# Performance work log

Hardware: AMD Instinct MI355X
Metric: run time of the kernel (lower is better)

Reference implementation:

```python
import jax, jax.numpy as jnp
import numpy as np

N = 50000      # nodes
E = 800000     # edges (avg degree 16)
IN = 64        # in_channels
OUT = 64       # out_channels
K = 3          # Chebyshev order
LAM = 2.0      # lambda_max for sym normalization


def setup_inputs() -> dict:
    key = jax.random.key(0)
    ks = jax.random.split(key, 16)
    s_in = 1.0 / np.sqrt(IN)
    s_out = 1.0 / np.sqrt(OUT)
    inp = {
        "X": jax.random.normal(ks[0], (N, IN), jnp.float32),
        "edge_index": jax.random.randint(ks[1], (2, E), 0, N, dtype=jnp.int64),
        "edge_weight": jax.random.uniform(ks[2], (E,), jnp.float32),
        # six ChebConv weight stacks [K, in, out] and biases [out]
        "W_xz": jax.random.normal(ks[3], (K, IN, OUT), jnp.float32) * s_in,
        "W_hz": jax.random.normal(ks[4], (K, OUT, OUT), jnp.float32) * s_out,
        "W_xr": jax.random.normal(ks[5], (K, IN, OUT), jnp.float32) * s_in,
        "W_hr": jax.random.normal(ks[6], (K, OUT, OUT), jnp.float32) * s_out,
        "W_xh": jax.random.normal(ks[7], (K, IN, OUT), jnp.float32) * s_in,
        "W_hh": jax.random.normal(ks[8], (K, OUT, OUT), jnp.float32) * s_out,
        "b_xz": jnp.zeros((OUT,), jnp.float32),
        "b_hz": jnp.zeros((OUT,), jnp.float32),
        "b_xr": jnp.zeros((OUT,), jnp.float32),
        "b_hr": jnp.zeros((OUT,), jnp.float32),
        "b_xh": jnp.zeros((OUT,), jnp.float32),
        "b_hh": jnp.zeros((OUT,), jnp.float32),
    }
    return inp


def _cheb_norm(edge_index, edge_weight):
    # PyG ChebConv __norm__ with sym normalization, lambda_max = 2:
    # L_hat = (2/lam) * (I - D^-1/2 A D^-1/2) - I
    src, dst = edge_index[0], edge_index[1]
    deg = jax.ops.segment_sum(edge_weight, src, num_segments=N)
    dinv = jnp.where(deg > 0, jax.lax.rsqrt(jnp.where(deg > 0, deg, 1.0)), 0.0)
    w_off = -(2.0 / LAM) * edge_weight * dinv[src] * dinv[dst]
    diag = 2.0 / LAM - 1.0  # 0 when lambda_max == 2
    return src, dst, w_off, diag


def _spmm(x, src, dst, w_off, diag):
    # y[i] = sum_{e: dst[e]=i} w_off[e] * x[src[e]] + diag * x[i]
    msg = w_off[:, None] * x[src]
    return jax.ops.segment_sum(msg, dst, num_segments=N) + diag * x


def _cheb_conv(x, W, b, src, dst, w_off, diag):
    Tx0 = x
    out = Tx0 @ W[0]
    Tx1 = _spmm(Tx0, src, dst, w_off, diag)
    out = out + Tx1 @ W[1]
    for k in range(2, K):
        Tx2 = 2.0 * _spmm(Tx1, src, dst, w_off, diag) - Tx0
        out = out + Tx2 @ W[k]
        Tx0, Tx1 = Tx1, Tx2
    return out + b


def reference(X, edge_index, edge_weight,
              W_xz, W_hz, W_xr, W_hr, W_xh, W_hh,
              b_xz, b_hz, b_xr, b_hr, b_xh, b_hh):
    src, dst, w_off, diag = _cheb_norm(edge_index, edge_weight)
    cheb = lambda x, W, b: _cheb_conv(x, W, b, src, dst, w_off, diag)
    H = jnp.zeros((N, OUT), X.dtype)  # _set_hidden_state with H=None
    Z = jax.nn.sigmoid(cheb(X, W_xz, b_xz) + cheb(H, W_hz, b_hz))
    R = jax.nn.sigmoid(cheb(X, W_xr, b_xr) + cheb(H, W_hr, b_hr))
    H_tilde = jnp.tanh(cheb(X, W_xh, b_xh) + cheb(H * R, W_hh, b_hh))
    H_new = Z * H + (1.0 - Z) * H_tilde
    return H_new
```

## Files before the change

### kernel.cpp

```cpp
#include <hip/hip_runtime.h>


#define N_NODES 50000
#define E_EDGES 800000
#define NC 64
#define BSH 6
#define BUKN 64
#define NBUK 782
#define EPB 2048
#define NBLK 391

#define OFF_CV       0
#define OFF_ROWSTART 1600000
#define OFF_TOTD     1650016
#define OFF_BASED    1650800
#define OFF_TOTS     1651584
#define OFF_BASES    1652368
#define OFF_TX1      1653152
#define OFF_RECD     1653152
#define OFF_DINV     3253152
#define OFF_CNTD     3303168
#define OFF_TX2      4853152
#define OFF_RECS     4853152
#define OFF_CNTS     6453152
#define OFF_WB       8053152

typedef __attribute__((ext_vector_type(8))) short bf16x8;
typedef __attribute__((ext_vector_type(4))) float f32x4;

__device__ __forceinline__ unsigned bf16rne(float x) {
    unsigned u = __float_as_uint(x);
    return (u + 0x7fffu + ((u >> 16) & 1u)) >> 16;
}

__global__ __launch_bounds__(256) void k_hist(const int* __restrict__ ei,
        int* __restrict__ cntD, int* __restrict__ cntS,
        const float* __restrict__ Wz, const float* __restrict__ Wh,
        short* __restrict__ WB) {
    int t = threadIdx.x, blk = blockIdx.x;
    if (blk >= NBLK) {
        int mg = blk - NBLK;
        int m = mg >> 1, g = mg & 1;
        const float* W = (g ? Wh : Wz) + m * 4096;
        #pragma unroll
        for (int r = 0; r < 16; ++r) {
            int idx = r * 256 + t;
            int c = idx >> 6, o = idx & 63;
            float x = W[idx];
            unsigned hi = bf16rne(x);
            float fhi = __uint_as_float(hi << 16);
            unsigned lo = bf16rne(x - fhi);
            WB[(mg * 2 + 0) * 4096 + o * 64 + c] = (short)hi;
            WB[(mg * 2 + 1) * 4096 + o * 64 + c] = (short)lo;
        }
        return;
    }
    __shared__ int hD[NBUK], hS[NBUK];
    for (int b = t; b < NBUK; b += 256) { hD[b] = 0; hS[b] = 0; }
    __syncthreads();
    int e0 = blk * EPB;
    #pragma unroll
    for (int i = 0; i < 8; ++i) {
        int e = e0 + i * 256 + t;
        if (e < E_EDGES) {
            atomicAdd(&hS[ei[e] >> BSH], 1);
            atomicAdd(&hD[ei[E_EDGES + e] >> BSH], 1);
        }
    }
    __syncthreads();
    for (int b = t; b < NBUK; b += 256) {
        cntD[b * NBLK + blk] = hD[b];
        cntS[b * NBLK + blk] = hS[b];
    }
}

__global__ __launch_bounds__(256) void k_scanPB(int* __restrict__ cntD,
        int* __restrict__ cntS, int* __restrict__ totD, int* __restrict__ totS) {
    __shared__ int s[512];
    int t = threadIdx.x;
    int row = blockIdx.x; int* cnt; int* tot;
    if (row < NBUK) { cnt = cntD; tot = totD; }
    else            { row -= NBUK; cnt = cntS; tot = totS; }
    int v0 = (t < NBLK) ? cnt[row * NBLK + t] : 0;
    int v1 = (256 + t < NBLK) ? cnt[row * NBLK + 256 + t] : 0;
    s[t] = v0; s[256 + t] = v1;
    __syncthreads();
    for (int off = 1; off < 512; off <<= 1) {
        int a = (t >= off) ? s[t - off] : 0;
        int b = (256 + t >= off) ? s[256 + t - off] : 0;
        __syncthreads();
        s[t] += a; s[256 + t] += b;
        __syncthreads();
    }
    if (t < NBLK) cnt[row * NBLK + t] = s[t] - v0;
    if (256 + t < NBLK) cnt[row * NBLK + 256 + t] = s[256 + t] - v1;
    if (t == 0) tot[row] = s[511];
}

__global__ __launch_bounds__(256) void k_scanTot(int* __restrict__ totD,
        int* __restrict__ baseD, int* __restrict__ totS, int* __restrict__ baseS) {
    __shared__ int s[1024];
    int t = threadIdx.x;
    int* tot  = blockIdx.x ? totS  : totD;
    int* base = blockIdx.x ? baseS : baseD;
    int v[4];
    #pragma unroll
    for (int q = 0; q < 4; ++q) {
        int i = q * 256 + t;
        v[q] = (i < NBUK) ? tot[i] : 0;
        s[i] = v[q];
    }
    __syncthreads();
    for (int off = 1; off < 1024; off <<= 1) {
        int a[4];
        #pragma unroll
        for (int q = 0; q < 4; ++q) {
            int i = q * 256 + t;
            a[q] = (i >= off) ? s[i - off] : 0;
        }
        __syncthreads();
        #pragma unroll
        for (int q = 0; q < 4; ++q) s[q * 256 + t] += a[q];
        __syncthreads();
    }
    #pragma unroll
    for (int q = 0; q < 4; ++q) {
        int i = q * 256 + t;
        if (i < NBUK) base[i] = s[i] - v[q];
    }
}

__global__ __launch_bounds__(256) void k_scatter(const int* __restrict__ ei,
        const float* __restrict__ ew, const int* __restrict__ offD,
        const int* __restrict__ offS, const int* __restrict__ baseD,
        const int* __restrict__ baseS, long long* __restrict__ recD,
        long long* __restrict__ recS) {
    __shared__ int curD[NBUK], curS[NBUK];
    int t = threadIdx.x, blk = blockIdx.x;
    for (int b = t; b < NBUK; b += 256) {
        curD[b] = baseD[b] + offD[b * NBLK + blk];
        curS[b] = baseS[b] + offS[b * NBLK + blk];
    }
    __syncthreads();
    int e0 = blk * EPB;
    #pragma unroll
    for (int i = 0; i < 8; ++i) {
        int e = e0 + i * 256 + t;
        if (e < E_EDGES) {
            int sN = ei[e], dN = ei[E_EDGES + e];
            long long wb = (long long)(unsigned)__float_as_uint(ew[e]) << 32;
            int pD = atomicAdd(&curD[dN >> BSH], 1);
            recD[pD] = wb | (unsigned)((sN << BSH) | (dN & (BUKN - 1)));
            int pS = atomicAdd(&curS[sN >> BSH], 1);
            recS[pS] = wb | (unsigned)(sN & (BUKN - 1));
        }
    }
}

__global__ __launch_bounds__(256) void k_deg(const long long* __restrict__ recS,
        const int* __restrict__ totS, const int* __restrict__ baseS,
        float* __restrict__ dinv) {
    __shared__ float degL[BUKN];
    int t = threadIdx.x, b = blockIdx.x;
    if (t < BUKN) degL[t] = 0.f;
    __syncthreads();
    int st = baseS[b], n = totS[b];
    for (int i = t; i < n; i += 256) {
        long long r = recS[st + i];
        atomicAdd(&degL[(int)(r & (BUKN - 1))], __uint_as_float((unsigned)(r >> 32)));
    }
    __syncthreads();
    if (t < BUKN) {
        int node = b * BUKN + t;
        if (node < N_NODES) {
            float dg = degL[t];
            dinv[node] = dg > 0.f ? rsqrtf(dg) : 0.f;
        }
    }
}

__global__ __launch_bounds__(256) void k_csr(const long long* __restrict__ recD,
        const int* __restrict__ totD, const int* __restrict__ baseD,
        const float* __restrict__ dinv, long long* __restrict__ cv,
        int* __restrict__ row_start) {
    __shared__ int cnt[BUKN], cur[BUKN];
    __shared__ float dL[BUKN];
    int t = threadIdx.x, b = blockIdx.x;
    if (t < BUKN) {
        cnt[t] = 0;
        int node = b * BUKN + t;
        dL[t] = (node < N_NODES) ? dinv[node] : 0.f;
    }
    __syncthreads();
    int st = baseD[b], n = totD[b];
    for (int i = t; i < n; i += 256)
        atomicAdd(&cnt[(int)(recD[st + i] & (BUKN - 1))], 1);
    __syncthreads();
    if (t < BUKN) {
        int x = cnt[t];
        int orig = x;
        #pragma unroll
        for (int off = 1; off < BUKN; off <<= 1) {
            int v = __shfl_up(x, off, 64);
            if ((t & 63) >= off) x += v;
        }
        cur[t] = x - orig;
        int node = b * BUKN + t;
        if (node < N_NODES) row_start[node] = st + (x - orig);
    }
    if (b == 0 && t == 0) row_start[N_NODES] = E_EDGES;
    __syncthreads();
    for (int i = t; i < n; i += 256) {
        long long r = recD[st + i];
        int m = (int)(r & 0xffffffffLL);
        float w = __uint_as_float((unsigned)(r >> 32));
        int rr = m & (BUKN - 1);
        int sN = m >> BSH;
        float val = -w * dinv[sN] * dL[rr];
        int pos = st + atomicAdd(&cur[rr], 1);
        cv[pos] = ((long long)__float_as_int(val) << 32) | (unsigned)sN;
    }
}

template<int SCALE, int SUB>
__global__ __launch_bounds__(256) void k_spmm(
        const int* __restrict__ row_start, const long long* __restrict__ cv,
        const float* __restrict__ xin, const float* __restrict__ xprev,
        float* __restrict__ out) {
    int wid = (blockIdx.x << 2) + (threadIdx.x >> 6);
    int l = threadIdx.x & 63;
    if (wid >= N_NODES) return;
    int start = row_start[wid];
    int end   = row_start[wid + 1];
    int sub = l >> 4;
    int q   = l & 15;
    float4 acc = make_float4(0.f, 0.f, 0.f, 0.f);
    for (int j = start; j < end; j += 8) {
        int jA = j + sub;
        int jB = j + 4 + sub;
        long long pA = (jA < end) ? cv[jA] : 0LL;
        long long pB = (jB < end) ? cv[jB] : 0LL;
        float4 xA = *(const float4*)&xin[(size_t)(unsigned)(pA & 0xffffffffLL) * NC + q * 4];
        float4 xB = *(const float4*)&xin[(size_t)(unsigned)(pB & 0xffffffffLL) * NC + q * 4];
        float vA = __int_as_float((int)(pA >> 32));
        float vB = __int_as_float((int)(pB >> 32));
        acc.x = fmaf(vA, xA.x, acc.x);
        acc.y = fmaf(vA, xA.y, acc.y);
        acc.z = fmaf(vA, xA.z, acc.z);
        acc.w = fmaf(vA, xA.w, acc.w);
        acc.x = fmaf(vB, xB.x, acc.x);
        acc.y = fmaf(vB, xB.y, acc.y);
        acc.z = fmaf(vB, xB.z, acc.z);
        acc.w = fmaf(vB, xB.w, acc.w);
    }
    #pragma unroll
    for (int m = 16; m <= 32; m <<= 1) {
        acc.x += __shfl_xor(acc.x, m, 64);
        acc.y += __shfl_xor(acc.y, m, 64);
        acc.z += __shfl_xor(acc.z, m, 64);
        acc.w += __shfl_xor(acc.w, m, 64);
    }
    if (sub == 0) {
        float4 r;
        r.x = (float)SCALE * acc.x;
        r.y = (float)SCALE * acc.y;
        r.z = (float)SCALE * acc.z;
        r.w = (float)SCALE * acc.w;
        if (SUB) {
            float4 xo = *(const float4*)&xprev[(size_t)wid * NC + q * 4];
            r.x -= xo.x; r.y -= xo.y; r.z -= xo.z; r.w -= xo.w;
        }
        *(float4*)&out[(size_t)wid * NC + q * 4] = r;
    }
}

__global__ __launch_bounds__(256) void k_gru(
        const float* __restrict__ X, const float* __restrict__ Tx1,
        const float* __restrict__ Tx2, const short* __restrict__ WB,
        const float* __restrict__ bxz, const float* __restrict__ bhz,
        const float* __restrict__ bxh, const float* __restrict__ bhh,
        float* __restrict__ out) {
    __shared__ short Ahi[64 * 64];
    __shared__ short Alo[64 * 64];
    int tid = threadIdx.x;
    int l = tid & 63;
    int w = tid >> 6;
    int node0 = blockIdx.x * 64;

    f32x4 accz[4], acch[4];
    #pragma unroll
    for (int mt = 0; mt < 4; ++mt) {
        accz[mt] = (f32x4){0.f, 0.f, 0.f, 0.f};
        acch[mt] = (f32x4){0.f, 0.f, 0.f, 0.f};
    }

    const float* ins[3] = {X, Tx1, Tx2};
    #pragma unroll 1
    for (int m = 0; m < 3; ++m) {
        __syncthreads();
        const float* ip = ins[m];
        #pragma unroll
        for (int r = 0; r < 4; ++r) {
            int fidx = r * 256 + tid;
            int n = fidx >> 4, c4 = fidx & 15;
            int gn = node0 + n;
            float4 v = make_float4(0.f, 0.f, 0.f, 0.f);
            if (gn < N_NODES) v = *(const float4*)&ip[(size_t)gn * 64 + c4 * 4];
            unsigned h0 = bf16rne(v.x), h1 = bf16rne(v.y),
                     h2 = bf16rne(v.z), h3 = bf16rne(v.w);
            unsigned q0 = bf16rne(v.x - __uint_as_float(h0 << 16));
            unsigned q1 = bf16rne(v.y - __uint_as_float(h1 << 16));
            unsigned q2 = bf16rne(v.z - __uint_as_float(h2 << 16));
            unsigned q3 = bf16rne(v.w - __uint_as_float(h3 << 16));
            int kk = (c4 * 4) ^ ((n & 7) << 3);
            *(uint2*)&Ahi[n * 64 + kk] = make_uint2(h0 | (h1 << 16), h2 | (h3 << 16));
            *(uint2*)&Alo[n * 64 + kk] = make_uint2(q0 | (q1 << 16), q2 | (q3 << 16));
        }
        __syncthreads();
        const short* wbm = WB + m * 4 * 4096;
        #pragma unroll
        for (int kt = 0; kt < 2; ++kt) {
            int k0 = kt * 32 + (l >> 4) * 8;
            bf16x8 ah[4], al[4];
            #pragma unroll
            for (int mt = 0; mt < 4; ++mt) {
                int row = mt * 16 + (l & 15);
                int kk = k0 ^ ((row & 7) << 3);
                ah[mt] = *(const bf16x8*)&Ahi[row * 64 + kk];
                al[mt] = *(const bf16x8*)&Alo[row * 64 + kk];
            }
            int o = w * 16 + (l & 15);
            {
                bf16x8 bh_ = *(const bf16x8*)&wbm[0 * 4096 + o * 64 + k0];
                bf16x8 bl_ = *(const bf16x8*)&wbm[1 * 4096 + o * 64 + k0];
                #pragma unroll
                for (int mt = 0; mt < 4; ++mt) {
                    accz[mt] = __builtin_amdgcn_mfma_f32_16x16x32_bf16(ah[mt], bh_, accz[mt], 0, 0, 0);
                    accz[mt] = __builtin_amdgcn_mfma_f32_16x16x32_bf16(ah[mt], bl_, accz[mt], 0, 0, 0);
                    accz[mt] = __builtin_amdgcn_mfma_f32_16x16x32_bf16(al[mt], bh_, accz[mt], 0, 0, 0);
                }
            }
            {
                bf16x8 bh_ = *(const bf16x8*)&wbm[2 * 4096 + o * 64 + k0];
                bf16x8 bl_ = *(const bf16x8*)&wbm[3 * 4096 + o * 64 + k0];
                #pragma unroll
                for (int mt = 0; mt < 4; ++mt) {
                    acch[mt] = __builtin_amdgcn_mfma_f32_16x16x32_bf16(ah[mt], bh_, acch[mt], 0, 0, 0);
                    acch[mt] = __builtin_amdgcn_mfma_f32_16x16x32_bf16(ah[mt], bl_, acch[mt], 0, 0, 0);
                    acch[mt] = __builtin_amdgcn_mfma_f32_16x16x32_bf16(al[mt], bh_, acch[mt], 0, 0, 0);
                }
            }
        }
    }

    int o = w * 16 + (l & 15);
    float bz = bxz[o] + bhz[o];
    float bh = bxh[o] + bhh[o];
    #pragma unroll
    for (int mt = 0; mt < 4; ++mt) {
        #pragma unroll
        for (int r = 0; r < 4; ++r) {
            int node = node0 + mt * 16 + (l >> 4) * 4 + r;
            if (node < N_NODES) {
                float z = accz[mt][r] + bz;
                float h = acch[mt][r] + bh;
                float sig = 1.f / (1.f + __expf(-z));
                float e2 = __expf(-2.f * h);
                float th = (1.f - e2) / (1.f + e2);
                out[(size_t)node * 64 + o] = (1.f - sig) * th;
            }
        }
    }
}

extern "C" void kernel_launch(void* const* d_in, const int* in_sizes, int n_in,
                              void* d_out, int out_size, void* d_ws, size_t ws_size,
                              hipStream_t stream) {
    const float* X   = (const float*)d_in[0];
    const int*   ei  = (const int*)d_in[1];
    const float* ew  = (const float*)d_in[2];
    const float* Wxz = (const float*)d_in[3];
    const float* Wxh = (const float*)d_in[7];
    const float* bxz = (const float*)d_in[9];
    const float* bhz = (const float*)d_in[10];
    const float* bxh = (const float*)d_in[13];
    const float* bhh = (const float*)d_in[14];
    float* out = (float*)d_out;

    float* ws_f = (float*)d_ws;
    int*   ws_i = (int*)d_ws;

    long long* cv       = (long long*)(ws_i + OFF_CV);
    int*       rowstart = ws_i + OFF_ROWSTART;
    int*       totD     = ws_i + OFF_TOTD;
    int*       baseD    = ws_i + OFF_BASED;
    int*       totS     = ws_i + OFF_TOTS;
    int*       baseS    = ws_i + OFF_BASES;
    float*     tx1      = ws_f + OFF_TX1;
    long long* recD     = (long long*)(ws_i + OFF_RECD);
    float*     dinv     = ws_f + OFF_DINV;
    int*       cntD     = ws_i + OFF_CNTD;
    float*     tx2      = ws_f + OFF_TX2;
    long long* recS     = (long long*)(ws_i + OFF_RECS);
    int*       cntS     = ws_i + OFF_CNTS;
    short*     WB       = (short*)(ws_i + OFF_WB);

    const int TB = 256;
    k_hist<<<NBLK + 6, TB, 0, stream>>>(ei, cntD, cntS, Wxz, Wxh, WB);
    k_scanPB<<<2 * NBUK, TB, 0, stream>>>(cntD, cntS, totD, totS);
    k_scanTot<<<2, TB, 0, stream>>>(totD, baseD, totS, baseS);
    k_scatter<<<NBLK, TB, 0, stream>>>(ei, ew, cntD, cntS, baseD, baseS, recD, recS);
    k_deg<<<NBUK, TB, 0, stream>>>(recS, totS, baseS, dinv);
    k_csr<<<NBUK, TB, 0, stream>>>(recD, totD, baseD, dinv, cv, rowstart);

    k_spmm<1, 0><<<(N_NODES + 3) / 4, TB, 0, stream>>>(rowstart, cv, X, X, tx1);
    k_spmm<2, 1><<<(N_NODES + 3) / 4, TB, 0, stream>>>(rowstart, cv, tx1, X, tx2);

    k_gru<<<NBUK, TB, 0, stream>>>(X, tx1, tx2, WB, bxz, bhz, bxh, bhh, out);
}
```

Measured before the change: 147.1 us.

## Factor degree normalization out of CSR and pre-split bf16 operands in producers

Stores raw edge weights in the CSR and applies the D^-1/2 scaling algebraically: the source side is prescaled (xs = dinv*X, u1 = dinv*Tx1) and the destination side is applied at the end of each SpMM row, so k_csr no longer does random dinv gathers. The hi/lo bf16 split of X, Tx1 and Tx2 moves into the producing kernels (k_degx, k_spmm), and k_gru now reads those pre-split operands straight from global memory instead of converting through LDS with barriers. k_csr also caches bucket records in LDS to avoid rereading them. The cost is extra workspace and extra global writes for the split arrays and prescaled copies, and the MFMA A-operand loads in k_gru become strided global reads.

```diff
diff --git a/kernel.cpp b/kernel.cpp
--- a/kernel.cpp
+++ b/kernel.cpp
@@ -7,8 +7,10 @@
 #define BSH 6
 #define BUKN 64
 #define NBUK 782
+#define NPADROW 50048
 #define EPB 2048
 #define NBLK 391
+#define CSR_CAP 1536
 
 #define OFF_CV       0
 #define OFF_ROWSTART 1600000
@@ -16,14 +18,20 @@
 #define OFF_BASED    1650800
 #define OFF_TOTS     1651584
 #define OFF_BASES    1652368
-#define OFF_TX1      1653152
-#define OFF_RECD     1653152
-#define OFF_DINV     3253152
-#define OFF_CNTD     3303168
-#define OFF_TX2      4853152
-#define OFF_RECS     4853152
-#define OFF_CNTS     6453152
-#define OFF_WB       8053152
+#define OFF_XS       1653152
+#define OFF_U1       4853152
+#define OFF_RECD     8053152
+#define OFF_RECS     9653152
+#define OFF_DINV     11253152
+#define OFF_CNTD     11303200
+#define OFF_CNTS     11608962
+#define OFF_WB       11914724
+#define OFF_XHI      11939300
+#define OFF_XLO      13540836
+#define OFF_T1HI     15142372
+#define OFF_T1LO     16743908
+#define OFF_T2HI     18345444
+#define OFF_T2LO     19946980
 
 typedef __attribute__((ext_vector_type(8))) short bf16x8;
 typedef __attribute__((ext_vector_type(4))) float f32x4;
@@ -157,10 +165,11 @@
     }
 }
 
-__global__ __launch_bounds__(256) void k_deg(const long long* __restrict__ recS,
+__global__ __launch_bounds__(256) void k_degx(const long long* __restrict__ recS,
         const int* __restrict__ totS, const int* __restrict__ baseS,
-        float* __restrict__ dinv) {
-    __shared__ float degL[BUKN];
+        const float* __restrict__ X, float* __restrict__ dinv,
+        float* __restrict__ xs, short* __restrict__ xhi, short* __restrict__ xlo) {
+    __shared__ float degL[BUKN], dinvL[BUKN];
     int t = threadIdx.x, b = blockIdx.x;
     if (t < BUKN) degL[t] = 0.f;
     __syncthreads();
@@ -172,29 +181,50 @@
     __syncthreads();
     if (t < BUKN) {
         int node = b * BUKN + t;
-        if (node < N_NODES) {
-            float dg = degL[t];
-            dinv[node] = dg > 0.f ? rsqrtf(dg) : 0.f;
-        }
+        float dg = degL[t];
+        float dv = (node < N_NODES && dg > 0.f) ? rsqrtf(dg) : 0.f;
+        dinvL[t] = dv;
+        if (node < N_NODES) dinv[node] = dv;
+    }
+    __syncthreads();
+    #pragma unroll
+    for (int it = 0; it < 4; ++it) {
+        int fidx = it * 256 + t;
+        int rl = fidx >> 4, c4 = fidx & 15;
+        int gn = b * BUKN + rl;
+        float4 v = make_float4(0.f, 0.f, 0.f, 0.f);
+        if (gn < N_NODES) v = *(const float4*)&X[(size_t)gn * 64 + c4 * 4];
+        float dv = dinvL[rl];
+        if (gn < N_NODES) {
+            float4 sv = make_float4(dv * v.x, dv * v.y, dv * v.z, dv * v.w);
+            *(float4*)&xs[(size_t)gn * 64 + c4 * 4] = sv;
+        }
+        unsigned h0 = bf16rne(v.x), h1 = bf16rne(v.y),
+                 h2 = bf16rne(v.z), h3 = bf16rne(v.w);
+        unsigned q0 = bf16rne(v.x - __uint_as_float(h0 << 16));
+        unsigned q1 = bf16rne(v.y - __uint_as_float(h1 << 16));
+        unsigned q2 = bf16rne(v.z - __uint_as_float(h2 << 16));
+        unsigned q3 = bf16rne(v.w - __uint_as_float(h3 << 16));
+        *(uint2*)&xhi[(size_t)gn * 64 + c4 * 4] = make_uint2(h0 | (h1 << 16), h2 | (h3 << 16));
+        *(uint2*)&xlo[(size_t)gn * 64 + c4 * 4] = make_uint2(q0 | (q1 << 16), q2 | (q3 << 16));
     }
 }
 
 __global__ __launch_bounds__(256) void k_csr(const long long* __restrict__ recD,
         const int* __restrict__ totD, const int* __restrict__ baseD,
-        const float* __restrict__ dinv, long long* __restrict__ cv,
-        int* __restrict__ row_start) {
+        long long* __restrict__ cv, int* __restrict__ row_start) {
+    __shared__ long long recL[CSR_CAP];
     __shared__ int cnt[BUKN], cur[BUKN];
-    __shared__ float dL[BUKN];
     int t = threadIdx.x, b = blockIdx.x;
-    if (t < BUKN) {
-        cnt[t] = 0;
-        int node = b * BUKN + t;
-        dL[t] = (node < N_NODES) ? dinv[node] : 0.f;
-    }
+    if (t < BUKN) cnt[t] = 0;
     __syncthreads();
     int st = baseD[b], n = totD[b];
-    for (int i = t; i < n; i += 256)
-        atomicAdd(&cnt[(int)(recD[st + i] & (BUKN - 1))], 1);
+    bool fits = (n <= CSR_CAP);
+    for (int i = t; i < n; i += 256) {
+        long long r = recD[st + i];
+        if (fits) recL[i] = r;
+        atomicAdd(&cnt[(int)(r & (BUKN - 1))], 1);
+    }
     __syncthreads();
     if (t < BUKN) {
         int x = cnt[t];
@@ -211,22 +241,21 @@
     if (b == 0 && t == 0) row_start[N_NODES] = E_EDGES;
     __syncthreads();
     for (int i = t; i < n; i += 256) {
-        long long r = recD[st + i];
+        long long r = fits ? recL[i] : recD[st + i];
         int m = (int)(r & 0xffffffffLL);
-        float w = __uint_as_float((unsigned)(r >> 32));
         int rr = m & (BUKN - 1);
         int sN = m >> BSH;
-        float val = -w * dinv[sN] * dL[rr];
         int pos = st + atomicAdd(&cur[rr], 1);
-        cv[pos] = ((long long)__float_as_int(val) << 32) | (unsigned)sN;
-    }
-}
-
-template<int SCALE, int SUB>
+        cv[pos] = (r & 0xffffffff00000000LL) | (unsigned)sN;
+    }
+}
+
+template<int PASS>
 __global__ __launch_bounds__(256) void k_spmm(
         const int* __restrict__ row_start, const long long* __restrict__ cv,
-        const float* __restrict__ xin, const float* __restrict__ xprev,
-        float* __restrict__ out) {
+        const float* __restrict__ gsrc, const float* __restrict__ X,
+        const float* __restrict__ dinv, float* __restrict__ u1,
+        short* __restrict__ phi, short* __restrict__ plo) {
     int wid = (blockIdx.x << 2) + (threadIdx.x >> 6);
     int l = threadIdx.x & 63;
     if (wid >= N_NODES) return;
@@ -235,23 +264,20 @@
     int sub = l >> 4;
     int q   = l & 15;
     float4 acc = make_float4(0.f, 0.f, 0.f, 0.f);
+    #pragma unroll 2
     for (int j = start; j < end; j += 8) {
         int jA = j + sub;
         int jB = j + 4 + sub;
         long long pA = (jA < end) ? cv[jA] : 0LL;
         long long pB = (jB < end) ? cv[jB] : 0LL;
-        float4 xA = *(const float4*)&xin[(size_t)(unsigned)(pA & 0xffffffffLL) * NC + q * 4];
-        float4 xB = *(const float4*)&xin[(size_t)(unsigned)(pB & 0xffffffffLL) * NC + q * 4];
+        float4 xA = *(const float4*)&gsrc[(size_t)(unsigned)(pA & 0xffffffffLL) * NC + q * 4];
+        float4 xB = *(const float4*)&gsrc[(size_t)(unsigned)(pB & 0xffffffffLL) * NC + q * 4];
         float vA = __int_as_float((int)(pA >> 32));
         float vB = __int_as_float((int)(pB >> 32));
-        acc.x = fmaf(vA, xA.x, acc.x);
-        acc.y = fmaf(vA, xA.y, acc.y);
-        acc.z = fmaf(vA, xA.z, acc.z);
-        acc.w = fmaf(vA, xA.w, acc.w);
-        acc.x = fmaf(vB, xB.x, acc.x);
-        acc.y = fmaf(vB, xB.y, acc.y);
-        acc.z = fmaf(vB, xB.z, acc.z);
-        acc.w = fmaf(vB, xB.w, acc.w);
+        acc.x = fmaf(vA, xA.x, acc.x); acc.y = fmaf(vA, xA.y, acc.y);
+        acc.z = fmaf(vA, xA.z, acc.z); acc.w = fmaf(vA, xA.w, acc.w);
+        acc.x = fmaf(vB, xB.x, acc.x); acc.y = fmaf(vB, xB.y, acc.y);
+        acc.z = fmaf(vB, xB.z, acc.z); acc.w = fmaf(vB, xB.w, acc.w);
     }
     #pragma unroll
     for (int m = 16; m <= 32; m <<= 1) {
@@ -261,27 +287,37 @@
         acc.w += __shfl_xor(acc.w, m, 64);
     }
     if (sub == 0) {
+        float dv = dinv[wid];
         float4 r;
-        r.x = (float)SCALE * acc.x;
-        r.y = (float)SCALE * acc.y;
-        r.z = (float)SCALE * acc.z;
-        r.w = (float)SCALE * acc.w;
-        if (SUB) {
-            float4 xo = *(const float4*)&xprev[(size_t)wid * NC + q * 4];
-            r.x -= xo.x; r.y -= xo.y; r.z -= xo.z; r.w -= xo.w;
-        }
-        *(float4*)&out[(size_t)wid * NC + q * 4] = r;
+        if (PASS == 1) {
+            r.x = -dv * acc.x; r.y = -dv * acc.y;
+            r.z = -dv * acc.z; r.w = -dv * acc.w;
+            *(float4*)&u1[(size_t)wid * NC + q * 4] =
+                make_float4(dv * r.x, dv * r.y, dv * r.z, dv * r.w);
+        } else {
+            const float4 xo = *(const float4*)&X[(size_t)wid * NC + q * 4];
+            r.x = -2.f * dv * acc.x - xo.x; r.y = -2.f * dv * acc.y - xo.y;
+            r.z = -2.f * dv * acc.z - xo.z; r.w = -2.f * dv * acc.w - xo.w;
+        }
+        unsigned h0 = bf16rne(r.x), h1 = bf16rne(r.y),
+                 h2 = bf16rne(r.z), h3 = bf16rne(r.w);
+        unsigned q0 = bf16rne(r.x - __uint_as_float(h0 << 16));
+        unsigned q1 = bf16rne(r.y - __uint_as_float(h1 << 16));
+        unsigned q2 = bf16rne(r.z - __uint_as_float(h2 << 16));
+        unsigned q3 = bf16rne(r.w - __uint_as_float(h3 << 16));
+        *(uint2*)&phi[(size_t)wid * NC + q * 4] = make_uint2(h0 | (h1 << 16), h2 | (h3 << 16));
+        *(uint2*)&plo[(size_t)wid * NC + q * 4] = make_uint2(q0 | (q1 << 16), q2 | (q3 << 16));
     }
 }
 
 __global__ __launch_bounds__(256) void k_gru(
-        const float* __restrict__ X, const float* __restrict__ Tx1,
-        const float* __restrict__ Tx2, const short* __restrict__ WB,
+        const short* __restrict__ xhi, const short* __restrict__ xlo,
+        const short* __restrict__ t1hi, const short* __restrict__ t1lo,
+        const short* __restrict__ t2hi, const short* __restrict__ t2lo,
+        const short* __restrict__ WB,
         const float* __restrict__ bxz, const float* __restrict__ bhz,
         const float* __restrict__ bxh, const float* __restrict__ bhh,
         float* __restrict__ out) {
-    __shared__ short Ahi[64 * 64];
-    __shared__ short Alo[64 * 64];
     int tid = threadIdx.x;
     int l = tid & 63;
     int w = tid >> 6;
@@ -294,29 +330,14 @@
         acch[mt] = (f32x4){0.f, 0.f, 0.f, 0.f};
     }
 
-    const float* ins[3] = {X, Tx1, Tx2};
-    #pragma unroll 1
+    const short* PHI[3] = {xhi, t1hi, t2hi};
+    const short* PLO[3] = {xlo, t1lo, t2lo};
+    int o = w * 16 + (l & 15);
+
+    #pragma unroll
     for (int m = 0; m < 3; ++m) {
-        __syncthreads();
-        const float* ip = ins[m];
-        #pragma unroll
-        for (int r = 0; r < 4; ++r) {
-            int fidx = r * 256 + tid;
-            int n = fidx >> 4, c4 = fidx & 15;
-            int gn = node0 + n;
-            float4 v = make_float4(0.f, 0.f, 0.f, 0.f);
-            if (gn < N_NODES) v = *(const float4*)&ip[(size_t)gn * 64 + c4 * 4];
-            unsigned h0 = bf16rne(v.x), h1 = bf16rne(v.y),
-                     h2 = bf16rne(v.z), h3 = bf16rne(v.w);
-            unsigned q0 = bf16rne(v.x - __uint_as_float(h0 << 16));
-            unsigned q1 = bf16rne(v.y - __uint_as_float(h1 << 16));
-            unsigned q2 = bf16rne(v.z - __uint_as_float(h2 << 16));
-            unsigned q3 = bf16rne(v.w - __uint_as_float(h3 << 16));
-            int kk = (c4 * 4) ^ ((n & 7) << 3);
-            *(uint2*)&Ahi[n * 64 + kk] = make_uint2(h0 | (h1 << 16), h2 | (h3 << 16));
-            *(uint2*)&Alo[n * 64 + kk] = make_uint2(q0 | (q1 << 16), q2 | (q3 << 16));
-        }
-        __syncthreads();
+        const short* phi = PHI[m];
+        const short* plo = PLO[m];
         const short* wbm = WB + m * 4 * 4096;
         #pragma unroll
         for (int kt = 0; kt < 2; ++kt) {
@@ -324,36 +345,26 @@
             bf16x8 ah[4], al[4];
             #pragma unroll
             for (int mt = 0; mt < 4; ++mt) {
-                int row = mt * 16 + (l & 15);
-                int kk = k0 ^ ((row & 7) << 3);
-                ah[mt] = *(const bf16x8*)&Ahi[row * 64 + kk];
-                al[mt] = *(const bf16x8*)&Alo[row * 64 + kk];
+                size_t rowoff = (size_t)(node0 + mt * 16 + (l & 15)) * 64 + k0;
+                ah[mt] = *(const bf16x8*)&phi[rowoff];
+                al[mt] = *(const bf16x8*)&plo[rowoff];
             }
-            int o = w * 16 + (l & 15);
-            {
-                bf16x8 bh_ = *(const bf16x8*)&wbm[0 * 4096 + o * 64 + k0];
-                bf16x8 bl_ = *(const bf16x8*)&wbm[1 * 4096 + o * 64 + k0];
-                #pragma unroll
-                for (int mt = 0; mt < 4; ++mt) {
-                    accz[mt] = __builtin_amdgcn_mfma_f32_16x16x32_bf16(ah[mt], bh_, accz[mt], 0, 0, 0);
-                    accz[mt] = __builtin_amdgcn_mfma_f32_16x16x32_bf16(ah[mt], bl_, accz[mt], 0, 0, 0);
-                    accz[mt] = __builtin_amdgcn_mfma_f32_16x16x32_bf16(al[mt], bh_, accz[mt], 0, 0, 0);
-                }
+            bf16x8 bzh = *(const bf16x8*)&wbm[0 * 4096 + o * 64 + k0];
+            bf16x8 bzl = *(const bf16x8*)&wbm[1 * 4096 + o * 64 + k0];
+            bf16x8 bhh_ = *(const bf16x8*)&wbm[2 * 4096 + o * 64 + k0];
+            bf16x8 bhl = *(const bf16x8*)&wbm[3 * 4096 + o * 64 + k0];
+            #pragma unroll
+            for (int mt = 0; mt < 4; ++mt) {
+                accz[mt] = __builtin_amdgcn_mfma_f32_16x16x32_bf16(ah[mt], bzh, accz[mt], 0, 0, 0);
+                accz[mt] = __builtin_amdgcn_mfma_f32_16x16x32_bf16(ah[mt], bzl, accz[mt], 0, 0, 0);
+                accz[mt] = __builtin_amdgcn_mfma_f32_16x16x32_bf16(al[mt], bzh, accz[mt], 0, 0, 0);
+                acch[mt] = __builtin_amdgcn_mfma_f32_16x16x32_bf16(ah[mt], bhh_, acch[mt], 0, 0, 0);
+                acch[mt] = __builtin_amdgcn_mfma_f32_16x16x32_bf16(ah[mt], bhl, acch[mt], 0, 0, 0);
+                acch[mt] = __builtin_amdgcn_mfma_f32_16x16x32_bf16(al[mt], bhh_, acch[mt], 0, 0, 0);
             }
-            {
-                bf16x8 bh_ = *(const bf16x8*)&wbm[2 * 4096 + o * 64 + k0];
-                bf16x8 bl_ = *(const bf16x8*)&wbm[3 * 4096 + o * 64 + k0];
-                #pragma unroll
-                for (int mt = 0; mt < 4; ++mt) {
-                    acch[mt] = __builtin_amdgcn_mfma_f32_16x16x32_bf16(ah[mt], bh_, acch[mt], 0, 0, 0);
-                    acch[mt] = __builtin_amdgcn_mfma_f32_16x16x32_bf16(ah[mt], bl_, acch[mt], 0, 0, 0);
-                    acch[mt] = __builtin_amdgcn_mfma_f32_16x16x32_bf16(al[mt], bh_, acch[mt], 0, 0, 0);
-                }
-            }
-        }
-    }
-
-    int o = w * 16 + (l & 15);
+        }
+    }
+
     float bz = bxz[o] + bhz[o];
     float bh = bxh[o] + bhh[o];
     #pragma unroll
@@ -387,8 +398,8 @@
     const float* bhh = (const float*)d_in[14];
     float* out = (float*)d_out;
 
+    int* ws_i = (int*)d_ws;
     float* ws_f = (float*)d_ws;
-    int*   ws_i = (int*)d_ws;
 
     long long* cv       = (long long*)(ws_i + OFF_CV);
     int*       rowstart = ws_i + OFF_ROWSTART;
@@ -396,25 +407,32 @@
     int*       baseD    = ws_i + OFF_BASED;
     int*       totS     = ws_i + OFF_TOTS;
     int*       baseS    = ws_i + OFF_BASES;
-    float*     tx1      = ws_f + OFF_TX1;
+    float*     xs       = ws_f + OFF_XS;
+    float*     u1       = ws_f + OFF_U1;
     long long* recD     = (long long*)(ws_i + OFF_RECD);
+    long long* recS     = (long long*)(ws_i + OFF_RECS);
     float*     dinv     = ws_f + OFF_DINV;
     int*       cntD     = ws_i + OFF_CNTD;
-    float*     tx2      = ws_f + OFF_TX2;
-    long long* recS     = (long long*)(ws_i + OFF_RECS);
     int*       cntS     = ws_i + OFF_CNTS;
     short*     WB       = (short*)(ws_i + OFF_WB);
+    short*     xhi      = (short*)(ws_i + OFF_XHI);
+    short*     xlo      = (short*)(ws_i + OFF_XLO);
+    short*     t1hi     = (short*)(ws_i + OFF_T1HI);
+    short*     t1lo     = (short*)(ws_i + OFF_T1LO);
+    short*     t2hi     = (short*)(ws_i + OFF_T2HI);
+    short*     t2lo     = (short*)(ws_i + OFF_T2LO);
 
     const int TB = 256;
     k_hist<<<NBLK + 6, TB, 0, stream>>>(ei, cntD, cntS, Wxz, Wxh, WB);
     k_scanPB<<<2 * NBUK, TB, 0, stream>>>(cntD, cntS, totD, totS);
     k_scanTot<<<2, TB, 0, stream>>>(totD, baseD, totS, baseS);
     k_scatter<<<NBLK, TB, 0, stream>>>(ei, ew, cntD, cntS, baseD, baseS, recD, recS);
-    k_deg<<<NBUK, TB, 0, stream>>>(recS, totS, baseS, dinv);
-    k_csr<<<NBUK, TB, 0, stream>>>(recD, totD, baseD, dinv, cv, rowstart);
-
-    k_spmm<1, 0><<<(N_NODES + 3) / 4, TB, 0, stream>>>(rowstart, cv, X, X, tx1);
-    k_spmm<2, 1><<<(N_NODES + 3) / 4, TB, 0, stream>>>(rowstart, cv, tx1, X, tx2);
-
-    k_gru<<<NBUK, TB, 0, stream>>>(X, tx1, tx2, WB, bxz, bhz, bxh, bhh, out);
-}
+    k_degx<<<NBUK, TB, 0, stream>>>(recS, totS, baseS, X, dinv, xs, xhi, xlo);
+    k_csr<<<NBUK, TB, 0, stream>>>(recD, totD, baseD, cv, rowstart);
+
+    k_spmm<1><<<(N_NODES + 3) / 4, TB, 0, stream>>>(rowstart, cv, xs, X, dinv, u1, t1hi, t1lo);
+    k_spmm<2><<<(N_NODES + 3) / 4, TB, 0, stream>>>(rowstart, cv, u1, X, dinv, u1, t2hi, t2lo);
+
+    k_gru<<<NBUK, TB, 0, stream>>>(xhi, xlo, t1hi, t1lo, t2hi, t2lo, WB,
+                                   bxz, bhz, bxh, bhh, out);
+}
```

After: 167.9 us. 1.14x slower.

## Restructure GRU kernel to 32-node tiles with all inputs loaded upfront

Applied to the files above, without the earlier changes.

The GRU projection kernel now handles 32 nodes per block instead of 64, doubling the grid. It loads X, Tx1 and Tx2 into registers before any conversion and stages all three into shared memory with a single barrier, rather than looping with two barriers per input. It also unrolls the SpMM edge loop by two to get more gathers in flight. The aim is more parallelism and memory-level overlap in the final GEMM stage, paid for with more register pressure, more shared memory per block, and weight fragments reloaded by twice as many blocks.

```diff
diff --git a/kernel.cpp b/kernel.cpp
--- a/kernel.cpp
+++ b/kernel.cpp
@@ -9,6 +9,7 @@
 #define NBUK 782
 #define EPB 2048
 #define NBLK 391
+#define GRUB 1563
 
 #define OFF_CV       0
 #define OFF_ROWSTART 1600000
@@ -235,6 +236,7 @@
     int sub = l >> 4;
     int q   = l & 15;
     float4 acc = make_float4(0.f, 0.f, 0.f, 0.f);
+    #pragma unroll 2
     for (int j = start; j < end; j += 8) {
         int jA = j + sub;
         int jB = j + 4 + sub;
@@ -244,14 +246,10 @@
         float4 xB = *(const float4*)&xin[(size_t)(unsigned)(pB & 0xffffffffLL) * NC + q * 4];
         float vA = __int_as_float((int)(pA >> 32));
         float vB = __int_as_float((int)(pB >> 32));
-        acc.x = fmaf(vA, xA.x, acc.x);
-        acc.y = fmaf(vA, xA.y, acc.y);
-        acc.z = fmaf(vA, xA.z, acc.z);
-        acc.w = fmaf(vA, xA.w, acc.w);
-        acc.x = fmaf(vB, xB.x, acc.x);
-        acc.y = fmaf(vB, xB.y, acc.y);
-        acc.z = fmaf(vB, xB.z, acc.z);
-        acc.w = fmaf(vB, xB.w, acc.w);
+        acc.x = fmaf(vA, xA.x, acc.x); acc.y = fmaf(vA, xA.y, acc.y);
+        acc.z = fmaf(vA, xA.z, acc.z); acc.w = fmaf(vA, xA.w, acc.w);
+        acc.x = fmaf(vB, xB.x, acc.x); acc.y = fmaf(vB, xB.y, acc.y);
+        acc.z = fmaf(vB, xB.z, acc.z); acc.w = fmaf(vB, xB.w, acc.w);
     }
     #pragma unroll
     for (int m = 16; m <= 32; m <<= 1) {
@@ -280,84 +278,92 @@
         const float* __restrict__ bxz, const float* __restrict__ bhz,
         const float* __restrict__ bxh, const float* __restrict__ bhh,
         float* __restrict__ out) {
-    __shared__ short Ahi[64 * 64];
-    __shared__ short Alo[64 * 64];
+    __shared__ short Ahi[3 * 32 * 64];
+    __shared__ short Alo[3 * 32 * 64];
     int tid = threadIdx.x;
     int l = tid & 63;
     int w = tid >> 6;
-    int node0 = blockIdx.x * 64;
-
-    f32x4 accz[4], acch[4];
-    #pragma unroll
-    for (int mt = 0; mt < 4; ++mt) {
-        accz[mt] = (f32x4){0.f, 0.f, 0.f, 0.f};
-        acch[mt] = (f32x4){0.f, 0.f, 0.f, 0.f};
-    }
+    int node0 = blockIdx.x * 32;
 
     const float* ins[3] = {X, Tx1, Tx2};
-    #pragma unroll 1
+
+    float4 v[3][2];
+    #pragma unroll
     for (int m = 0; m < 3; ++m) {
-        __syncthreads();
         const float* ip = ins[m];
         #pragma unroll
-        for (int r = 0; r < 4; ++r) {
+        for (int r = 0; r < 2; ++r) {
             int fidx = r * 256 + tid;
             int n = fidx >> 4, c4 = fidx & 15;
             int gn = node0 + n;
-            float4 v = make_float4(0.f, 0.f, 0.f, 0.f);
-            if (gn < N_NODES) v = *(const float4*)&ip[(size_t)gn * 64 + c4 * 4];
-            unsigned h0 = bf16rne(v.x), h1 = bf16rne(v.y),
-                     h2 = bf16rne(v.z), h3 = bf16rne(v.w);
-            unsigned q0 = bf16rne(v.x - __uint_as_float(h0 << 16));
-            unsigned q1 = bf16rne(v.y - __uint_as_float(h1 << 16));
-            unsigned q2 = bf16rne(v.z - __uint_as_float(h2 << 16));
-            unsigned q3 = bf16rne(v.w - __uint_as_float(h3 << 16));
+            v[m][r] = (gn < N_NODES) ? *(const float4*)&ip[(size_t)gn * 64 + c4 * 4]
+                                     : make_float4(0.f, 0.f, 0.f, 0.f);
+        }
+    }
+    #pragma unroll
+    for (int m = 0; m < 3; ++m) {
+        #pragma unroll
+        for (int r = 0; r < 2; ++r) {
+            int fidx = r * 256 + tid;
+            int n = fidx >> 4, c4 = fidx & 15;
+            float4 x = v[m][r];
+            unsigned h0 = bf16rne(x.x), h1 = bf16rne(x.y),
+                     h2 = bf16rne(x.z), h3 = bf16rne(x.w);
+            unsigned q0 = bf16rne(x.x - __uint_as_float(h0 << 16));
+            unsigned q1 = bf16rne(x.y - __uint_as_float(h1 << 16));
+            unsigned q2 = bf16rne(x.z - __uint_as_float(h2 << 16));
+            unsigned q3 = bf16rne(x.w - __uint_as_float(h3 << 16));
             int kk = (c4 * 4) ^ ((n & 7) << 3);
-            *(uint2*)&Ahi[n * 64 + kk] = make_uint2(h0 | (h1 << 16), h2 | (h3 << 16));
-            *(uint2*)&Alo[n * 64 + kk] = make_uint2(q0 | (q1 << 16), q2 | (q3 << 16));
-        }
-        __syncthreads();
+            int base = (m * 32 + n) * 64 + kk;
+            *(uint2*)&Ahi[base] = make_uint2(h0 | (h1 << 16), h2 | (h3 << 16));
+            *(uint2*)&Alo[base] = make_uint2(q0 | (q1 << 16), q2 | (q3 << 16));
+        }
+    }
+    __syncthreads();
+
+    f32x4 accz[2], acch[2];
+    #pragma unroll
+    for (int mt = 0; mt < 2; ++mt) {
+        accz[mt] = (f32x4){0.f, 0.f, 0.f, 0.f};
+        acch[mt] = (f32x4){0.f, 0.f, 0.f, 0.f};
+    }
+    int o = w * 16 + (l & 15);
+
+    #pragma unroll
+    for (int m = 0; m < 3; ++m) {
         const short* wbm = WB + m * 4 * 4096;
         #pragma unroll
         for (int kt = 0; kt < 2; ++kt) {
             int k0 = kt * 32 + (l >> 4) * 8;
-            bf16x8 ah[4], al[4];
+            bf16x8 ah[2], al[2];
             #pragma unroll
-            for (int mt = 0; mt < 4; ++mt) {
+            for (int mt = 0; mt < 2; ++mt) {
                 int row = mt * 16 + (l & 15);
                 int kk = k0 ^ ((row & 7) << 3);
-                ah[mt] = *(const bf16x8*)&Ahi[row * 64 + kk];
-                al[mt] = *(const bf16x8*)&Alo[row * 64 + kk];
+                int base = (m * 32 + row) * 64 + kk;
+                ah[mt] = *(const bf16x8*)&Ahi[base];
+                al[mt] = *(const bf16x8*)&Alo[base];
             }
-            int o = w * 16 + (l & 15);
-            {
-                bf16x8 bh_ = *(const bf16x8*)&wbm[0 * 4096 + o * 64 + k0];
-                bf16x8 bl_ = *(const bf16x8*)&wbm[1 * 4096 + o * 64 + k0];
-                #pragma unroll
-                for (int mt = 0; mt < 4; ++mt) {
-                    accz[mt] = __builtin_amdgcn_mfma_f32_16x16x32_bf16(ah[mt], bh_, accz[mt], 0, 0, 0);
-                    accz[mt] = __builtin_amdgcn_mfma_f32_16x16x32_bf16(ah[mt], bl_, accz[mt], 0, 0, 0);
-                    accz[mt] = __builtin_amdgcn_mfma_f32_16x16x32_bf16(al[mt], bh_, accz[mt], 0, 0, 0);
-                }
+            bf16x8 bzh = *(const bf16x8*)&wbm[0 * 4096 + o * 64 + k0];
+            bf16x8 bzl = *(const bf16x8*)&wbm[1 * 4096 + o * 64 + k0];
+            bf16x8 bhh_ = *(const bf16x8*)&wbm[2 * 4096 + o * 64 + k0];
+            bf16x8 bhl = *(const bf16x8*)&wbm[3 * 4096 + o * 64 + k0];
+            #pragma unroll
+            for (int mt = 0; mt < 2; ++mt) {
+                accz[mt] = __builtin_amdgcn_mfma_f32_16x16x32_bf16(ah[mt], bzh, accz[mt], 0, 0, 0);
+                accz[mt] = __builtin_amdgcn_mfma_f32_16x16x32_bf16(ah[mt], bzl, accz[mt], 0, 0, 0);
+                accz[mt] = __builtin_amdgcn_mfma_f32_16x16x32_bf16(al[mt], bzh, accz[mt], 0, 0, 0);
+                acch[mt] = __builtin_amdgcn_mfma_f32_16x16x32_bf16(ah[mt], bhh_, acch[mt], 0, 0, 0);
+                acch[mt] = __builtin_amdgcn_mfma_f32_16x16x32_bf16(ah[mt], bhl, acch[mt], 0, 0, 0);
+                acch[mt] = __builtin_amdgcn_mfma_f32_16x16x32_bf16(al[mt], bhh_, acch[mt], 0, 0, 0);
             }
-            {
-                bf16x8 bh_ = *(const bf16x8*)&wbm[2 * 4096 + o * 64 + k0];
-                bf16x8 bl_ = *(const bf16x8*)&wbm[3 * 4096 + o * 64 + k0];
-                #pragma unroll
-                for (int mt = 0; mt < 4; ++mt) {
-                    acch[mt] = __builtin_amdgcn_mfma_f32_16x16x32_bf16(ah[mt], bh_, acch[mt], 0, 0, 0);
-                    acch[mt] = __builtin_amdgcn_mfma_f32_16x16x32_bf16(ah[mt], bl_, acch[mt], 0, 0, 0);
-                    acch[mt] = __builtin_amdgcn_mfma_f32_16x16x32_bf16(al[mt], bh_, acch[mt], 0, 0, 0);
-                }
-            }
-        }
-    }
-
-    int o = w * 16 + (l & 15);
+        }
+    }
+
     float bz = bxz[o] + bhz[o];
     float bh = bxh[o] + bhh[o];
     #pragma unroll
-    for (int mt = 0; mt < 4; ++mt) {
+    for (int mt = 0; mt < 2; ++mt) {
         #pragma unroll
         for (int r = 0; r < 4; ++r) {
             int node = node0 + mt * 16 + (l >> 4) * 4 + r;
@@ -416,5 +422,5 @@
     k_spmm<1, 0><<<(N_NODES + 3) / 4, TB, 0, stream>>>(rowstart, cv, X, X, tx1);
     k_spmm<2, 1><<<(N_NODES + 3) / 4, TB, 0, stream>>>(rowstart, cv, tx1, X, tx2);
 
-    k_gru<<<NBUK, TB, 0, stream>>>(X, tx1, tx2, WB, bxz, bhz, bxh, bhh, out);
-}
+    k_gru<<<GRUB, TB, 0, stream>>>(X, tx1, tx2, WB, bxz, bhz, bxh, bhh, out);
+}
```

New measurement: 151.4 us. +2.9%, slower.

## Stage GRU inputs directly to LDS in fp32 and split to bf16 per fragment

Applied to the files above, without the earlier changes.

The GRU GEMM kernel now issues `global_load_lds` for all three inputs (X, Tx1, Tx2) at once into a swizzled fp32 LDS buffer, behind a single barrier. Before, it loaded, split into bf16 hi/lo and stored each input in turn, with barriers between the three passes. The bf16 hi/lo split now happens in registers when each wave reads its A fragments. The aim is to overlap global loads and remove the per-input barriers. In exchange, LDS use grows to 48KB per block, which can lower occupancy, and every wave now repeats the conversion work.

```diff
diff --git a/kernel.cpp b/kernel.cpp
--- a/kernel.cpp
+++ b/kernel.cpp
@@ -280,43 +280,43 @@
         const float* __restrict__ bxz, const float* __restrict__ bhz,
         const float* __restrict__ bxh, const float* __restrict__ bhh,
         float* __restrict__ out) {
-    __shared__ short Ahi[64 * 64];
-    __shared__ short Alo[64 * 64];
+    __shared__ float Alds[3 * 64 * 64];
     int tid = threadIdx.x;
     int l = tid & 63;
     int w = tid >> 6;
     int node0 = blockIdx.x * 64;
 
+    const float* ins[3] = {X, Tx1, Tx2};
+
+    #pragma unroll
+    for (int m = 0; m < 3; ++m) {
+        const float* ip = ins[m];
+        #pragma unroll
+        for (int it = 0; it < 4; ++it) {
+            int lg = w * 256 + it * 64 + l;
+            int n = lg >> 4, g = lg & 15;
+            int gs = g ^ ((n & 7) << 1);
+            int gn = node0 + n;
+            const float* src = ip + (size_t)gn * 64 + gs * 4;
+            float* dst = &Alds[m * 4096 + w * 1024 + it * 256];
+            if (gn < N_NODES)
+                __builtin_amdgcn_global_load_lds(
+                    (const __attribute__((address_space(1))) void*)src,
+                    (__attribute__((address_space(3))) void*)dst, 16, 0, 0);
+        }
+    }
+    __syncthreads();
+
     f32x4 accz[4], acch[4];
     #pragma unroll
     for (int mt = 0; mt < 4; ++mt) {
         accz[mt] = (f32x4){0.f, 0.f, 0.f, 0.f};
         acch[mt] = (f32x4){0.f, 0.f, 0.f, 0.f};
     }
-
-    const float* ins[3] = {X, Tx1, Tx2};
-    #pragma unroll 1
+    int o = w * 16 + (l & 15);
+
+    #pragma unroll
     for (int m = 0; m < 3; ++m) {
-        __syncthreads();
-        const float* ip = ins[m];
-        #pragma unroll
-        for (int r = 0; r < 4; ++r) {
-            int fidx = r * 256 + tid;
-            int n = fidx >> 4, c4 = fidx & 15;
-            int gn = node0 + n;
-            float4 v = make_float4(0.f, 0.f, 0.f, 0.f);
-            if (gn < N_NODES) v = *(const float4*)&ip[(size_t)gn * 64 + c4 * 4];
-            unsigned h0 = bf16rne(v.x), h1 = bf16rne(v.y),
-                     h2 = bf16rne(v.z), h3 = bf16rne(v.w);
-            unsigned q0 = bf16rne(v.x - __uint_as_float(h0 << 16));
-            unsigned q1 = bf16rne(v.y - __uint_as_float(h1 << 16));
-            unsigned q2 = bf16rne(v.z - __uint_as_float(h2 << 16));
-            unsigned q3 = bf16rne(v.w - __uint_as_float(h3 << 16));
-            int kk = (c4 * 4) ^ ((n & 7) << 3);
-            *(uint2*)&Ahi[n * 64 + kk] = make_uint2(h0 | (h1 << 16), h2 | (h3 << 16));
-            *(uint2*)&Alo[n * 64 + kk] = make_uint2(q0 | (q1 << 16), q2 | (q3 << 16));
-        }
-        __syncthreads();
         const short* wbm = WB + m * 4 * 4096;
         #pragma unroll
         for (int kt = 0; kt < 2; ++kt) {
@@ -325,11 +325,18 @@
             #pragma unroll
             for (int mt = 0; mt < 4; ++mt) {
                 int row = mt * 16 + (l & 15);
-                int kk = k0 ^ ((row & 7) << 3);
-                ah[mt] = *(const bf16x8*)&Ahi[row * 64 + kk];
-                al[mt] = *(const bf16x8*)&Alo[row * 64 + kk];
+                int g0 = (k0 >> 2) ^ ((row & 7) << 1);
+                const float* p = &Alds[m * 4096 + row * 64 + g0 * 4];
+                float4 fa = *(const float4*)p;
+                float4 fb = *(const float4*)(p + 4);
+                float f0[8] = {fa.x, fa.y, fa.z, fa.w, fb.x, fb.y, fb.z, fb.w};
+                #pragma unroll
+                for (int e = 0; e < 8; ++e) {
+                    unsigned hi = bf16rne(f0[e]);
+                    ah[mt][e] = (short)hi;
+                    al[mt][e] = (short)bf16rne(f0[e] - __uint_as_float(hi << 16));
+                }
             }
-            int o = w * 16 + (l & 15);
             {
                 bf16x8 bh_ = *(const bf16x8*)&wbm[0 * 4096 + o * 64 + k0];
                 bf16x8 bl_ = *(const bf16x8*)&wbm[1 * 4096 + o * 64 + k0];
@@ -353,7 +360,6 @@
         }
     }
 
-    int o = w * 16 + (l & 15);
     float bz = bxz[o] + bhz[o];
     float bh = bxh[o] + bhh[o];
     #pragma unroll
```

Result: slower. 150.2 us (+2.1%).
